# Performance work log

Measured on AMD Instinct MI355X. Metric: run time of the kernel, lower is better.

## Reference

```python
import jax, jax.numpy as jnp
import numpy as np

B = 64          # graphs per batch
N_NODES = 2000  # nodes per graph (model hyperparameter: FC2 in_features)
NF = 128        # node features
H = 8           # hidden_dim
OC = 8          # out_channels
NC = 2          # n_classes
DEG = 16        # avg degree
SLOPE = 0.01


def _lin_init(key, fan_in, fan_out):
    k1, k2 = jax.random.split(key)
    s = 1.0 / np.sqrt(fan_in)
    W = jax.random.uniform(k1, (fan_in, fan_out), jnp.float32, -s, s)
    b = jax.random.uniform(k2, (fan_out,), jnp.float32, -s, s)
    return W, b


def setup_inputs() -> dict:
    key = jax.random.key(0)
    ks = jax.random.split(key, 10)
    N = B * N_NODES
    E = N * DEG
    x = jax.random.normal(ks[0], (N, NF), jnp.float32)
    # graph-local random edges, offset per graph
    local = jax.random.randint(ks[1], (2, E), 0, N_NODES)
    off = jnp.repeat(jnp.arange(B, dtype=jnp.int64) * N_NODES, E // B)
    edge_index = (local + off[None, :]).astype(jnp.int64)
    batch = jnp.repeat(jnp.arange(B, dtype=jnp.int64), N_NODES)
    W1a, b1a = _lin_init(ks[2], NF, H)
    W1b, b1b = _lin_init(ks[3], H, H)
    W2a, b2a = _lin_init(ks[4], H, H)
    W2b, b2b = _lin_init(ks[5], H, OC)
    Wf1, bf1 = _lin_init(ks[6], OC, 1)
    Wf2, bf2 = _lin_init(ks[7], N_NODES, NC)
    return {"x": x, "edge_index": edge_index, "batch": batch,
            "W1a": W1a, "b1a": b1a, "W1b": W1b, "b1b": b1b,
            "W2a": W2a, "b2a": b2a, "W2b": W2b, "b2b": b2b,
            "Wf1": Wf1, "bf1": bf1, "Wf2": Wf2, "bf2": bf2}


def _lrelu(v):
    return jnp.where(v >= 0, v, SLOPE * v)


def _gin_conv(h, src, dst, Wa, ba, Wb, bb):
    N = h.shape[0]
    agg = jax.ops.segment_sum(h[src], dst, num_segments=N)  # sum_{j->i} h_j
    z = h + agg                                             # (1+eps)*h + agg, eps=0
    z = _lrelu(z @ Wa + ba)                                 # MLP linear1 + act
    return z @ Wb + bb                                      # MLP linear2 (plain last)


def reference(x, edge_index, batch, W1a, b1a, W1b, b1b, W2a, b2a, W2b, b2b,
              Wf1, bf1, Wf2, bf2):
    src, dst = edge_index[0], edge_index[1]
    h = _gin_conv(x, src, dst, W1a, b1a, W1b, b1b)
    h = _lrelu(h)  # inter-layer activation (dropout = identity at eval)
    h = _gin_conv(h, src, dst, W2a, b2a, W2b, b2b)  # [N, OC], no act after last conv
    bsz = h.shape[0] // N_NODES
    y = h.reshape(bsz, N_NODES, OC)
    y = _lrelu(y) @ Wf1 + bf1          # FC1 -> [B, n_nodes, 1]
    y = y.reshape(bsz, N_NODES)
    y = _lrelu(y) @ Wf2 + bf2          # FC2 -> [B, n_classes]
    return jax.nn.log_softmax(y, axis=1)
```

## Files before the change

kernel.cpp:

```cpp
#include <hip/hip_runtime.h>
#include <math.h>

#define NF 128
#define HD 8
#define NPG 2000
#define EPB 8000
#define LPB 8
#define LNPB 250
#define FNPB 64
#define SLOPE 0.01f

__device__ __forceinline__ float lrelu(float v) {
    return v > 0.0f ? v : SLOPE * v;
}
__device__ __forceinline__ unsigned short f2bf(float f) {
    unsigned int u = __float_as_uint(f);
    return (unsigned short)((u + 0x7FFFu + ((u >> 16) & 1u)) >> 16);
}
__device__ __forceinline__ float bfl(unsigned int p) {
    return __uint_as_float(p << 16);
}
__device__ __forceinline__ float bfh(unsigned int p) {
    return __uint_as_float(p & 0xFFFF0000u);
}
__device__ __forceinline__ void gload_lds16(const void* g, void* l) {
    __builtin_amdgcn_global_load_lds(
        (const __attribute__((address_space(1))) unsigned int*)g,
        (__attribute__((address_space(3))) unsigned int*)l, 16, 0, 0);
}

__global__ __launch_bounds__(512, 8) void k_featsort(
    const float* __restrict__ x, const float* __restrict__ W1a,
    const int* __restrict__ ei, unsigned short* __restrict__ t1b,
    unsigned short* __restrict__ gcolb, int* __restrict__ rpc,
    int N, int E, int NC)
{
    __shared__ union {
        struct { float tile[FNPB * NF]; float wl[8 * 132]; } f;
        struct { int cnt[NPG]; unsigned short srt[EPB];
                 int wtot[8]; int wpre[8]; } s;
    } sm;

    const int tid = threadIdx.x;
    const int lane = tid & 63;
    const int wv = tid >> 6;

    if ((int)blockIdx.x < NC) {
        const int b = blockIdx.x;
        const int g = b >> 2;
        const int nodeBase = g * NPG;
        const int e0 = b * EPB;

        for (int i = tid; i < NPG; i += 512) sm.s.cnt[i] = 0;
        __syncthreads();

        for (int e = e0 + tid; e < e0 + EPB; e += 512) {
            int dl = ei[E + e] - nodeBase;
            atomicAdd(&sm.s.cnt[dl], 1);
        }
        __syncthreads();

        int c0 = 0, c1 = 0, c2 = 0, c3 = 0;
        if (tid < 500) {
            c0 = sm.s.cnt[4 * tid];     c1 = sm.s.cnt[4 * tid + 1];
            c2 = sm.s.cnt[4 * tid + 2]; c3 = sm.s.cnt[4 * tid + 3];
        }
        int s = c0 + c1 + c2 + c3;
        int isc = s;
#pragma unroll
        for (int d = 1; d < 64; d <<= 1) {
            int o = __shfl_up(isc, d);
            if (lane >= d) isc += o;
        }
        if (lane == 63) sm.s.wtot[wv] = isc;
        __syncthreads();
        if (wv == 0) {
            int v = (lane < 8) ? sm.s.wtot[lane] : 0;
            int iv = v;
#pragma unroll
            for (int d = 1; d < 8; d <<= 1) {
                int o = __shfl_up(iv, d);
                if (lane >= d) iv += o;
            }
            if (lane < 8) sm.s.wpre[lane] = iv - v;
        }
        __syncthreads();
        int excl = isc - s + sm.s.wpre[wv];

        int* rpb = rpc + (size_t)b * (NPG + 1);
        if (tid < 500) {
            int o0 = excl, o1 = excl + c0, o2 = o1 + c1, o3 = o2 + c2;
            sm.s.cnt[4 * tid]     = o0; sm.s.cnt[4 * tid + 1] = o1;
            sm.s.cnt[4 * tid + 2] = o2; sm.s.cnt[4 * tid + 3] = o3;
            rpb[4 * tid]     = o0; rpb[4 * tid + 1] = o1;
            rpb[4 * tid + 2] = o2; rpb[4 * tid + 3] = o3;
        }
        if (tid == 0) rpb[NPG] = EPB;
        __syncthreads();

        for (int e = e0 + tid; e < e0 + EPB; e += 512) {
            int src = ei[e] - nodeBase;
            int dl = ei[E + e] - nodeBase;
            int pos = atomicAdd(&sm.s.cnt[dl], 1);
            sm.s.srt[pos] = (unsigned short)src;
        }
        __syncthreads();

        unsigned int* dst = (unsigned int*)(gcolb + (size_t)b * EPB);
        const unsigned int* ss = (const unsigned int*)sm.s.srt;
        for (int i = tid; i < EPB / 2; i += 512) dst[i] = ss[i];
    } else {
        const size_t base = (size_t)(blockIdx.x - NC) * FNPB;

#pragma unroll
        for (int i = 0; i < 2; ++i) {
            int idx = tid + i * 512;
            int wcol = idx >> 7;
            int wk   = idx & 127;
            sm.f.wl[wcol * 132 + wk] = W1a[wk * 8 + wcol];
        }

        const float* xg = x + base * NF;
        char* tb = (char*)sm.f.tile;
#pragma unroll
        for (int i = 0; i < 4; ++i) {
            int s = wv * 256 + i * 64 + lane;
            int n = s >> 5, j = s & 31;
            gload_lds16(xg + n * NF + ((j ^ (n & 7)) << 2), tb + s * 16);
        }
        __syncthreads();

        const int col   = tid & 7;
        const int khalf = (tid >> 3) & 1;
        const int np    = tid >> 4;
        const int n0    = np * 2;
        const int ex0 = n0 & 7, ex1 = (n0 + 1) & 7;

        const float*  tf = sm.f.tile;
        const float4* w4 = (const float4*)sm.f.wl;
        float acc0 = 0.0f, acc1 = 0.0f;
#pragma unroll 4
        for (int i = 0; i < 16; ++i) {
            int k4 = khalf * 16 + i;
            float4 r0 = *(const float4*)(tf + n0 * NF + ((k4 ^ ex0) << 2));
            float4 r1 = *(const float4*)(tf + (n0 + 1) * NF + ((k4 ^ ex1) << 2));
            float4 w  = w4[col * 33 + k4];
            acc0 += r0.x * w.x + r0.y * w.y + r0.z * w.z + r0.w * w.w;
            acc1 += r1.x * w.x + r1.y * w.y + r1.z * w.z + r1.w * w.w;
        }
        acc0 += __shfl_xor(acc0, 8);
        acc1 += __shfl_xor(acc1, 8);
        if (khalf == 0) {
            t1b[(base + n0) * HD + col]     = f2bf(acc0);
            t1b[(base + n0 + 1) * HD + col] = f2bf(acc1);
        }
    }
}

#define GATHER_CHUNK(P)                                                       \
    {                                                                         \
        int b0 = rs[P], cnt = re[P] - b0;                                     \
        int sl[8];                                                            \
        _Pragma("unroll")                                                     \
        for (int j = 0; j < 8; ++j) {                                         \
            int idx = (j < cnt) ? (b0 + j) : 0;                               \
            sl[j] = colp[P][idx];                                             \
        }                                                                     \
        _Pragma("unroll")                                                     \
        for (int j = 0; j < 8; ++j) {                                         \
            float w = (j < cnt) ? 1.0f : 0.0f;                                \
            uint4 v = tbl[sl[j]];                                             \
            a0 += w * bfl(v.x); a1 += w * bfh(v.x);                           \
            a2 += w * bfl(v.y); a3 += w * bfh(v.y);                           \
            a4 += w * bfl(v.z); a5 += w * bfh(v.z);                           \
            a6 += w * bfl(v.w); a7 += w * bfh(v.w);                           \
        }                                                                     \
        for (int e2 = b0 + 8; e2 < b0 + cnt; ++e2) {                          \
            uint4 v = tbl[colp[P][e2]];                                       \
            a0 += bfl(v.x); a1 += bfh(v.x);                                   \
            a2 += bfl(v.y); a3 += bfh(v.y);                                   \
            a4 += bfl(v.z); a5 += bfh(v.z);                                   \
            a6 += bfl(v.w); a7 += bfh(v.w);                                   \
        }                                                                     \
    }

__global__ __launch_bounds__(512) void k_l1(
    const unsigned short* __restrict__ t1b, const int* __restrict__ rpc,
    const unsigned short* __restrict__ gcolb, unsigned short* __restrict__ ub,
    const float* __restrict__ b1a, const float* __restrict__ W1b,
    const float* __restrict__ b1b, const float* __restrict__ W2a)
{
    __shared__ uint4 tbl[2048];
    __shared__ float wts[144];

    const int b = blockIdx.x;
    const int g = b >> 3;
    const int q = b & 7;
    const int tid = threadIdx.x;
    const int lane = tid & 63;
    const int wv = tid >> 6;

    if (tid < 144) {
        float v;
        if (tid < 8)       v = b1a[tid];
        else if (tid < 72) v = W1b[tid - 8];
        else if (tid < 80) v = b1b[tid - 72];
        else               v = W2a[tid - 80];
        wts[tid] = v;
    }

    {
        const uint4* src4 = (const uint4*)(t1b + (size_t)g * NPG * HD);
        char* tb = (char*)tbl;
#pragma unroll
        for (int i = 0; i < 4; ++i) {
            int s = wv * 256 + i * 64 + lane;
            gload_lds16(src4 + s, tb + s * 16);
        }
    }
    __syncthreads();

    if (tid < 2 * LNPB) {
        const int node = tid >> 1;
        const int half = tid & 1;
        const int nl = q * LNPB + node;
        int rs[2], re[2];
        const unsigned short* colp[2];
#pragma unroll
        for (int p = 0; p < 2; ++p) {
            int ch = half * 2 + p;
            const int* rpb = rpc + (size_t)((g << 2) + ch) * (NPG + 1);
            colp[p] = gcolb + (size_t)((g << 2) + ch) * EPB;
            rs[p] = rpb[nl]; re[p] = rpb[nl + 1];
        }
        float a0 = 0, a1 = 0, a2 = 0, a3 = 0, a4 = 0, a5 = 0, a6 = 0, a7 = 0;
        GATHER_CHUNK(0) GATHER_CHUNK(1)
        a0 += __shfl_xor(a0, 1); a1 += __shfl_xor(a1, 1);
        a2 += __shfl_xor(a2, 1); a3 += __shfl_xor(a3, 1);
        a4 += __shfl_xor(a4, 1); a5 += __shfl_xor(a5, 1);
        a6 += __shfl_xor(a6, 1); a7 += __shfl_xor(a7, 1);

        if (half == 0) {
            uint4 sv = tbl[nl];
            float z[HD];
            z[0] = lrelu(bfl(sv.x) + a0 + wts[0]); z[1] = lrelu(bfh(sv.x) + a1 + wts[1]);
            z[2] = lrelu(bfl(sv.y) + a2 + wts[2]); z[3] = lrelu(bfh(sv.y) + a3 + wts[3]);
            z[4] = lrelu(bfl(sv.z) + a4 + wts[4]); z[5] = lrelu(bfh(sv.z) + a5 + wts[5]);
            z[6] = lrelu(bfl(sv.w) + a6 + wts[6]); z[7] = lrelu(bfh(sv.w) + a7 + wts[7]);

            float h[HD];
#pragma unroll
            for (int j = 0; j < HD; ++j) {
                float acc = wts[72 + j];
#pragma unroll
                for (int c = 0; c < HD; ++c) acc += z[c] * wts[8 + c * HD + j];
                h[j] = lrelu(acc);
            }
            float uu[HD];
#pragma unroll
            for (int j = 0; j < HD; ++j) {
                float acc = 0.0f;
#pragma unroll
                for (int c = 0; c < HD; ++c) acc += h[c] * wts[80 + c * HD + j];
                uu[j] = acc;
            }
            uint4 pk;
            pk.x = (unsigned int)f2bf(uu[0]) | ((unsigned int)f2bf(uu[1]) << 16);
            pk.y = (unsigned int)f2bf(uu[2]) | ((unsigned int)f2bf(uu[3]) << 16);
            pk.z = (unsigned int)f2bf(uu[4]) | ((unsigned int)f2bf(uu[5]) << 16);
            pk.w = (unsigned int)f2bf(uu[6]) | ((unsigned int)f2bf(uu[7]) << 16);
            ((uint4*)ub)[(size_t)g * NPG + nl] = pk;
        }
    }
}

__global__ __launch_bounds__(512) void k_l2(
    const unsigned short* __restrict__ ub, const int* __restrict__ rpc,
    const unsigned short* __restrict__ gcolb,
    const float* __restrict__ b2a, const float* __restrict__ W2b,
    const float* __restrict__ b2b, const float* __restrict__ Wf1,
    const float* __restrict__ bf1, const float* __restrict__ Wf2,
    float* __restrict__ bparts)
{
    __shared__ uint4 tbl[2048];
    __shared__ float wts[89];
    __shared__ float red[16];

    const int b = blockIdx.x;
    const int g = b >> 3;
    const int q = b & 7;
    const int tid = threadIdx.x;
    const int lane = tid & 63;
    const int wv = tid >> 6;

    if (tid < 89) {
        float v;
        if (tid < 8)       v = b2a[tid];
        else if (tid < 72) v = W2b[tid - 8];
        else if (tid < 80) v = b2b[tid - 72];
        else if (tid < 88) v = Wf1[tid - 80];
        else               v = bf1[0];
        wts[tid] = v;
    }

    {
        const uint4* src4 = (const uint4*)(ub + (size_t)g * NPG * HD);
        char* tb = (char*)tbl;
#pragma unroll
        for (int i = 0; i < 4; ++i) {
            int s = wv * 256 + i * 64 + lane;
            gload_lds16(src4 + s, tb + s * 16);
        }
    }
    __syncthreads();

    float acc0 = 0.0f, acc1 = 0.0f;
    if (tid < 2 * LNPB) {
        const int node = tid >> 1;
        const int half = tid & 1;
        const int nl = q * LNPB + node;
        int rs[2], re[2];
        const unsigned short* colp[2];
#pragma unroll
        for (int p = 0; p < 2; ++p) {
            int ch = half * 2 + p;
            const int* rpb = rpc + (size_t)((g << 2) + ch) * (NPG + 1);
            colp[p] = gcolb + (size_t)((g << 2) + ch) * EPB;
            rs[p] = rpb[nl]; re[p] = rpb[nl + 1];
        }
        float a0 = 0, a1 = 0, a2 = 0, a3 = 0, a4 = 0, a5 = 0, a6 = 0, a7 = 0;
        GATHER_CHUNK(0) GATHER_CHUNK(1)
        a0 += __shfl_xor(a0, 1); a1 += __shfl_xor(a1, 1);
        a2 += __shfl_xor(a2, 1); a3 += __shfl_xor(a3, 1);
        a4 += __shfl_xor(a4, 1); a5 += __shfl_xor(a5, 1);
        a6 += __shfl_xor(a6, 1); a7 += __shfl_xor(a7, 1);

        if (half == 0) {
            uint4 sv = tbl[nl];
            float z[HD];
            z[0] = lrelu(bfl(sv.x) + a0 + wts[0]); z[1] = lrelu(bfh(sv.x) + a1 + wts[1]);
            z[2] = lrelu(bfl(sv.y) + a2 + wts[2]); z[3] = lrelu(bfh(sv.y) + a3 + wts[3]);
            z[4] = lrelu(bfl(sv.z) + a4 + wts[4]); z[5] = lrelu(bfh(sv.z) + a5 + wts[5]);
            z[6] = lrelu(bfl(sv.w) + a6 + wts[6]); z[7] = lrelu(bfh(sv.w) + a7 + wts[7]);

            float svl = wts[88];
#pragma unroll
            for (int j = 0; j < HD; ++j) {
                float acc = wts[72 + j];
#pragma unroll
                for (int c = 0; c < HD; ++c) acc += z[c] * wts[8 + c * HD + j];
                svl += lrelu(acc) * wts[80 + j];
            }
            float pf = lrelu(svl);
            float2 wf = *(const float2*)(Wf2 + (size_t)nl * 2);
            acc0 = pf * wf.x;
            acc1 = pf * wf.y;
        }
    }

#pragma unroll
    for (int off = 32; off > 0; off >>= 1) {
        acc0 += __shfl_down(acc0, off);
        acc1 += __shfl_down(acc1, off);
    }
    if (lane == 0) { red[wv * 2] = acc0; red[wv * 2 + 1] = acc1; }
    __syncthreads();

    if (tid == 0) {
        float y0 = 0.f, y1 = 0.f;
#pragma unroll
        for (int w = 0; w < 8; ++w) { y0 += red[w * 2]; y1 += red[w * 2 + 1]; }
        *(float2*)(bparts + (size_t)b * 2) = make_float2(y0, y1);
    }
}

__global__ __launch_bounds__(64) void k_fin(const float* __restrict__ bparts,
                                            const float* __restrict__ bf2,
                                            float* __restrict__ out, int Bn) {
    int g = threadIdx.x;
    if (g >= Bn) return;
    float y0 = bf2[0], y1 = bf2[1];
#pragma unroll
    for (int b = 0; b < LPB; ++b) {
        float2 v = *(const float2*)(bparts + (size_t)(g * LPB + b) * 2);
        y0 += v.x; y1 += v.y;
    }
    float m = fmaxf(y0, y1);
    float lse = m + logf(expf(y0 - m) + expf(y1 - m));
    out[g * 2 + 0] = y0 - lse;
    out[g * 2 + 1] = y1 - lse;
}

extern "C" void kernel_launch(void* const* d_in, const int* in_sizes, int n_in,
                              void* d_out, int out_size, void* d_ws, size_t ws_size,
                              hipStream_t stream) {
    const float* x   = (const float*)d_in[0];
    const int*   ei  = (const int*)  d_in[1];
    const float* W1a = (const float*)d_in[3];
    const float* b1a = (const float*)d_in[4];
    const float* W1b = (const float*)d_in[5];
    const float* b1b = (const float*)d_in[6];
    const float* W2a = (const float*)d_in[7];
    const float* b2a = (const float*)d_in[8];
    const float* W2b = (const float*)d_in[9];
    const float* b2b = (const float*)d_in[10];
    const float* Wf1 = (const float*)d_in[11];
    const float* bf1 = (const float*)d_in[12];
    const float* Wf2 = (const float*)d_in[13];
    const float* bf2 = (const float*)d_in[14];

    int N   = in_sizes[0] / NF;
    int E   = in_sizes[1] / 2;
    int Bn  = N / NPG;
    int NC  = Bn * 4;

    unsigned short* t1b   = (unsigned short*)d_ws;
    unsigned short* ubuf  = t1b + (size_t)N * HD;
    unsigned short* gcolb = ubuf + (size_t)N * HD;
    int*            rpc   = (int*)(gcolb + (size_t)E);
    float*          bparts= (float*)(rpc + (size_t)NC * (NPG + 1) + 16);

    k_featsort<<<NC + N / FNPB, 512, 0, stream>>>(x, W1a, ei, t1b, gcolb, rpc,
                                                  N, E, NC);
    k_l1 <<<Bn * LPB, 512, 0, stream>>>(t1b, rpc, gcolb, ubuf, b1a, W1b, b1b, W2a);
    k_l2 <<<Bn * LPB, 512, 0, stream>>>(ubuf, rpc, gcolb, b2a, W2b, b2b, Wf1,
                                        bf1, Wf2, bparts);
    k_fin<<<1, 64, 0, stream>>>(bparts, bf2, (float*)d_out, Bn);
}
```

Before: 152.6 us.

## Fuse final log-softmax into layer-2 kernel via last-block atomic; double blocks per graph

Removes the separate final kernel launch. The last layer-2 block to finish is found with an atomic counter, which is reset in the first kernel, and that block does the per-graph reduction and log-softmax. Blocks per graph in both layer kernels go from 8 to 16, each covering half as many nodes, giving more parallelism across CUs. The cost is an extra fence and atomic per block, and each block now reloads the whole per-graph table for less work.

```diff
diff --git a/kernel.cpp b/kernel.cpp
--- a/kernel.cpp
+++ b/kernel.cpp
@@ -5,8 +5,8 @@
 #define HD 8
 #define NPG 2000
 #define EPB 8000
-#define LPB 8
-#define LNPB 250
+#define LPB 16
+#define LNPB 125
 #define FNPB 64
 #define SLOPE 0.01f
 
@@ -33,7 +33,7 @@
     const float* __restrict__ x, const float* __restrict__ W1a,
     const int* __restrict__ ei, unsigned short* __restrict__ t1b,
     unsigned short* __restrict__ gcolb, int* __restrict__ rpc,
-    int N, int E, int NC)
+    int* __restrict__ done, int N, int E, int NC)
 {
     __shared__ union {
         struct { float tile[FNPB * NF]; float wl[8 * 132]; } f;
@@ -47,6 +47,7 @@
 
     if ((int)blockIdx.x < NC) {
         const int b = blockIdx.x;
+        if (b == 0 && tid == 0) *done = 0;
         const int g = b >> 2;
         const int nodeBase = g * NPG;
         const int e0 = b * EPB;
@@ -194,8 +195,8 @@
     __shared__ float wts[144];
 
     const int b = blockIdx.x;
-    const int g = b >> 3;
-    const int q = b & 7;
+    const int g = b >> 4;
+    const int q = b & 15;
     const int tid = threadIdx.x;
     const int lane = tid & 63;
     const int wv = tid >> 6;
@@ -274,21 +275,23 @@
     }
 }
 
-__global__ __launch_bounds__(512) void k_l2(
+__global__ __launch_bounds__(512) void k_l2f(
     const unsigned short* __restrict__ ub, const int* __restrict__ rpc,
     const unsigned short* __restrict__ gcolb,
     const float* __restrict__ b2a, const float* __restrict__ W2b,
     const float* __restrict__ b2b, const float* __restrict__ Wf1,
     const float* __restrict__ bf1, const float* __restrict__ Wf2,
-    float* __restrict__ bparts)
+    const float* __restrict__ bf2, float* __restrict__ bparts,
+    int* __restrict__ done, float* __restrict__ out)
 {
     __shared__ uint4 tbl[2048];
     __shared__ float wts[89];
     __shared__ float red[16];
+    __shared__ int lastFlag;
 
     const int b = blockIdx.x;
-    const int g = b >> 3;
-    const int q = b & 7;
+    const int g = b >> 4;
+    const int q = b & 15;
     const int tid = threadIdx.x;
     const int lane = tid & 63;
     const int wv = tid >> 6;
@@ -371,24 +374,27 @@
 #pragma unroll
         for (int w = 0; w < 8; ++w) { y0 += red[w * 2]; y1 += red[w * 2 + 1]; }
         *(float2*)(bparts + (size_t)b * 2) = make_float2(y0, y1);
-    }
-}
-
-__global__ __launch_bounds__(64) void k_fin(const float* __restrict__ bparts,
-                                            const float* __restrict__ bf2,
-                                            float* __restrict__ out, int Bn) {
-    int g = threadIdx.x;
-    if (g >= Bn) return;
-    float y0 = bf2[0], y1 = bf2[1];
-#pragma unroll
-    for (int b = 0; b < LPB; ++b) {
-        float2 v = *(const float2*)(bparts + (size_t)(g * LPB + b) * 2);
-        y0 += v.x; y1 += v.y;
-    }
-    float m = fmaxf(y0, y1);
-    float lse = m + logf(expf(y0 - m) + expf(y1 - m));
-    out[g * 2 + 0] = y0 - lse;
-    out[g * 2 + 1] = y1 - lse;
+        __threadfence();
+        int prev = __hip_atomic_fetch_add(done, 1, __ATOMIC_ACQ_REL,
+                                          __HIP_MEMORY_SCOPE_AGENT);
+        lastFlag = (prev == (int)gridDim.x - 1);
+        if (lastFlag) __threadfence();
+    }
+    __syncthreads();
+
+    if (lastFlag && tid < 64) {
+        const int gg = tid;
+        float y0 = bf2[0], y1 = bf2[1];
+#pragma unroll
+        for (int p = 0; p < LPB; ++p) {
+            float2 v = *(const float2*)(bparts + (size_t)(gg * LPB + p) * 2);
+            y0 += v.x; y1 += v.y;
+        }
+        float m = fmaxf(y0, y1);
+        float lse = m + logf(expf(y0 - m) + expf(y1 - m));
+        out[gg * 2 + 0] = y0 - lse;
+        out[gg * 2 + 1] = y1 - lse;
+    }
 }
 
 extern "C" void kernel_launch(void* const* d_in, const int* in_sizes, int n_in,
@@ -419,11 +425,12 @@
     unsigned short* gcolb = ubuf + (size_t)N * HD;
     int*            rpc   = (int*)(gcolb + (size_t)E);
     float*          bparts= (float*)(rpc + (size_t)NC * (NPG + 1) + 16);
+    int*            done  = (int*)(bparts + 2048 + 16);
 
     k_featsort<<<NC + N / FNPB, 512, 0, stream>>>(x, W1a, ei, t1b, gcolb, rpc,
-                                                  N, E, NC);
+                                                  done, N, E, NC);
     k_l1 <<<Bn * LPB, 512, 0, stream>>>(t1b, rpc, gcolb, ubuf, b1a, W1b, b1b, W2a);
-    k_l2 <<<Bn * LPB, 512, 0, stream>>>(ubuf, rpc, gcolb, b2a, W2b, b2b, Wf1,
-                                        bf1, Wf2, bparts);
-    k_fin<<<1, 64, 0, stream>>>(bparts, bf2, (float*)d_out, Bn);
-}
+    k_l2f<<<Bn * LPB, 512, 0, stream>>>(ubuf, rpc, gcolb,
+                                        b2a, W2b, b2b, Wf1, bf1, Wf2, bf2,
+                                        bparts, done, (float*)d_out);
+}
```

Result: slower. 185.7 us (+21.7%).
